# Kernel tuning notes

Measured on AMD Instinct MI355X. Metric: run time of the kernel, lower is better.

## Reference

```python
import jax, jax.numpy as jnp
import numpy as np

B, S, D, E, K = 4, 2048, 2048, 64, 2

def setup_inputs() -> dict:
    key = jax.random.key(0)
    k1, k2, k3, k4 = jax.random.split(key, 4)
    x = jax.random.normal(k1, (B, S, D), dtype=jnp.float32)
    W = jax.random.normal(k2, (E, D), dtype=jnp.float32) * 0.02  # gate_linear.weight
    noise_weight = jax.random.normal(k3, (E,), dtype=jnp.float32) * 0.02
    noise = jax.random.normal(k4, (B, S, E), dtype=jnp.float32)  # torch.randn_like(logits), noisy_std=1.0
    return {"x": x, "W": W, "noise_weight": noise_weight, "noise": noise, "k": K}

def reference(x, W, noise_weight, noise, k):
    # logits = x @ W.T  -> [B, S, E]
    logits = jnp.einsum('bsd,ed->bse', x, W)
    # noise injection: randn * noisy_std(=1.0) * noise_weight (per-expert scale)
    logits_noisy = logits + noise * noise_weight
    # top-k over experts
    top_vals, top_idx = jax.lax.top_k(logits_noisy, k)  # [B, S, k]
    # softmax over a tensor that is -inf everywhere except the top-k slots is
    # exactly: zeros everywhere, softmax(top_vals) scattered into the top-k slots.
    probs = jax.nn.softmax(top_vals, axis=-1)  # [B, S, k]
    n_tok = B * S
    rows = jnp.arange(n_tok)[:, None]  # [n_tok, 1]
    gated = jnp.zeros((n_tok, E), dtype=logits.dtype)
    gated = gated.at[rows, top_idx.reshape(n_tok, k)].set(probs.reshape(n_tok, k))
    gated = gated.reshape(B, S, E)
    return gated, top_idx, top_vals
```

## Files before the change

### kernel.cpp

```cpp
#include <hip/hip_runtime.h>
#include <math.h>

#define NTOK 8192
#define DDIM 2048
#define NEXP 64
#define MT   16
#define ASTR 136
#define CSTR 68

#define GATED_SZ (NTOK * NEXP)
#define IDX_OFF  GATED_SZ
#define VALS_OFF (GATED_SZ + NTOK * 2)

#define NKSTEP (DDIM / 32)
#define NTILE  (NEXP / 16)
#define BFRAG_HALVES ((size_t)NKSTEP * NTILE * 64 * 8)

typedef _Float16 f16x8 __attribute__((ext_vector_type(8)));
typedef float    f32x4 __attribute__((ext_vector_type(4)));

__global__ void pack_b_kernel(const float* __restrict__ W,
                              _Float16* __restrict__ Bh,
                              _Float16* __restrict__ Bl)
{
    const int tid  = blockIdx.x * blockDim.x + threadIdx.x;
    const int lane = tid & 63;
    const int fid  = tid >> 6;
    const int ks   = fid >> 2;
    const int nt   = fid & 3;
    const int e    = nt * 16 + (lane & 15);
    const int k    = ks * 32 + (lane >> 4) * 8;
    const float* src = W + (size_t)e * DDIM + k;

    f16x8 hi, lo;
#pragma unroll
    for (int j = 0; j < 8; ++j) {
        const float v = src[j];
        const _Float16 h = (_Float16)v;
        hi[j] = h;
        lo[j] = (_Float16)((v - (float)h) * 4096.f);
    }
    *(f16x8*)(Bh + (size_t)tid * 8) = hi;
    *(f16x8*)(Bl + (size_t)tid * 8) = lo;
}

#define BFRAG(base, ks, nt) \
    (*(const f16x8*)((base) + ((((size_t)(ks)) * 4 + (nt)) * 64 + lane) * 8))

static __device__ __forceinline__ void cvt_hilo(float4 v0, float4 v1,
                                                f16x8& h8, f16x8& l8)
{
    const float vv[8] = {v0.x, v0.y, v0.z, v0.w, v1.x, v1.y, v1.z, v1.w};
#pragma unroll
    for (int j = 0; j < 8; ++j) {
        const _Float16 hh = (_Float16)vv[j];
        h8[j] = hh;
        l8[j] = (_Float16)((vv[j] - (float)hh) * 4096.f);
    }
}

__global__ __launch_bounds__(512, 4) void gate_kernel(
    const float* __restrict__ x,
    const _Float16* __restrict__ Bh,
    const _Float16* __restrict__ Bl,
    const float* __restrict__ noise_w,
    const float* __restrict__ noise,
    float* __restrict__ out)
{
    __shared__ _Float16 smem[8 * 2 * MT * ASTR];

    const int tid  = threadIdx.x;
    const int lane = tid & 63;
    const int w    = __builtin_amdgcn_readfirstlane(tid >> 6);
    const int tokBase = blockIdx.x * MT;

    const int q = lane >> 4;
    const int m = lane & 15;

    _Float16* xs = smem + (size_t)w * (2 * MT * ASTR);

    const float* xw = x + (size_t)tokBase * DDIM + (size_t)w * 256;

    f32x4 acc_hh[4], acc_lo[4];
#pragma unroll
    for (int nt = 0; nt < 4; ++nt) {
        acc_hh[nt] = (f32x4){0.f, 0.f, 0.f, 0.f};
        acc_lo[nt] = (f32x4){0.f, 0.f, 0.f, 0.f};
    }

#define LOADSUB(sc)                                                          \
    _Pragma("unroll")                                                        \
    for (int p = 0; p < 4; ++p) {                                            \
        const float* src = xw + (size_t)(p * 4 + q) * DDIM + (sc) * 128 + m * 8; \
        s0[p] = *(const float4*)(src);                                       \
        s1[p] = *(const float4*)(src + 4);                                   \
    }

#define STAGESUB()                                                           \
    _Pragma("unroll")                                                        \
    for (int p = 0; p < 4; ++p) {                                            \
        f16x8 h8, l8;                                                        \
        cvt_hilo(s0[p], s1[p], h8, l8);                                      \
        const int off = (p * 4 + q) * ASTR + m * 8;                          \
        *(f16x8*)&xs[off] = h8;                                              \
        *(f16x8*)&xs[MT * ASTR + off] = l8;                                  \
    }

#define COMPUTESUB(sc)                                                       \
    _Pragma("unroll")                                                        \
    for (int stp = 0; stp < 4; ++stp) {                                      \
        const int ks = w * 8 + (sc) * 4 + stp;                               \
        const f16x8 ah = *(const f16x8*)&xs[m * ASTR + stp * 32 + q * 8];    \
        const f16x8 al = *(const f16x8*)&xs[MT * ASTR + m * ASTR + stp * 32 + q * 8]; \
        _Pragma("unroll")                                                    \
        for (int nt = 0; nt < 4; ++nt) {                                     \
            const f16x8 bh = BFRAG(Bh, ks, nt);                              \
            const f16x8 bl = BFRAG(Bl, ks, nt);                              \
            acc_hh[nt] = __builtin_amdgcn_mfma_f32_16x16x32_f16(ah, bh, acc_hh[nt], 0, 0, 0); \
            acc_lo[nt] = __builtin_amdgcn_mfma_f32_16x16x32_f16(ah, bl, acc_lo[nt], 0, 0, 0); \
            acc_lo[nt] = __builtin_amdgcn_mfma_f32_16x16x32_f16(al, bh, acc_lo[nt], 0, 0, 0); \
        }                                                                    \
    }

    float4 s0[4], s1[4];
    LOADSUB(0)
    STAGESUB()
    LOADSUB(1)
    COMPUTESUB(0)
    STAGESUB()
    COMPUTESUB(1)

#undef LOADSUB
#undef STAGESUB
#undef COMPUTESUB

    __syncthreads();
    float* cbuf = (float*)smem;

#pragma unroll
    for (int nt = 0; nt < 4; ++nt) {
        const int e = nt * 16 + m;
#pragma unroll
        for (int r = 0; r < 4; ++r) {
            const int t = q * 4 + r;
            cbuf[((w * MT) + t) * CSTR + e] = acc_hh[nt][r] + acc_lo[nt][r] * (1.f / 4096.f);
        }
    }
    __syncthreads();

    const float nwv = noise_w[lane];
#pragma unroll
    for (int i = 0; i < 2; ++i) {
        const int t   = w * 2 + i;
        const int tok = tokBase + t;
        const int e   = lane;

        float v = 0.f;
#pragma unroll
        for (int p = 0; p < 8; ++p)
            v += cbuf[((p * MT) + t) * CSTR + e];
        v += noise[(size_t)tok * NEXP + e] * nwv;

        float m1 = v; int i1 = e;
#pragma unroll
        for (int sh = 32; sh > 0; sh >>= 1) {
            float ov = __shfl_xor(m1, sh, 64);
            int   oi = __shfl_xor(i1, sh, 64);
            if (ov > m1 || (ov == m1 && oi < i1)) { m1 = ov; i1 = oi; }
        }
        float vm = (e == i1) ? -INFINITY : v;
        float m2 = vm; int i2 = e;
#pragma unroll
        for (int sh = 32; sh > 0; sh >>= 1) {
            float ov = __shfl_xor(m2, sh, 64);
            int   oi = __shfl_xor(i2, sh, 64);
            if (ov > m2 || (ov == m2 && oi < i2)) { m2 = ov; i2 = oi; }
        }

        const float e2  = expf(m2 - m1);
        const float inv = 1.f / (1.f + e2);
        const float p1  = inv;
        const float p2  = e2 * inv;

        float gval = 0.f;
        if (e == i1) gval = p1;
        else if (e == i2) gval = p2;
        out[(size_t)tok * NEXP + e] = gval;

        if (lane == 0) {
            out[IDX_OFF  + tok * 2 + 0] = (float)i1;
            out[IDX_OFF  + tok * 2 + 1] = (float)i2;
            out[VALS_OFF + tok * 2 + 0] = m1;
            out[VALS_OFF + tok * 2 + 1] = m2;
        }
    }
}

extern "C" void kernel_launch(void* const* d_in, const int* in_sizes, int n_in,
                              void* d_out, int out_size, void* d_ws, size_t ws_size,
                              hipStream_t stream) {
    const float* x     = (const float*)d_in[0];
    const float* W     = (const float*)d_in[1];
    const float* nw    = (const float*)d_in[2];
    const float* noise = (const float*)d_in[3];
    float* out = (float*)d_out;

    _Float16* Bh = (_Float16*)d_ws;
    _Float16* Bl = Bh + BFRAG_HALVES;

    hipLaunchKernelGGL(pack_b_kernel, dim3(64), dim3(256), 0, stream, W, Bh, Bl);

    hipLaunchKernelGGL(gate_kernel, dim3(NTOK / MT), dim3(512), 0, stream,
                       x, Bh, Bl, nw, noise, out);
}
```

Baseline: 112.0 us.

## Halve per-wave LDS staging and deepen x prefetch to four sub-chunks

Each wave now stages its 256-element K slice in four 64-wide sub-chunks instead of two 128-wide ones. This cuts the LDS row stride from 136 to 72 halves and roughly halves the block's shared memory, so more blocks can be resident per CU. Two float4 register buffers alternate, so two global loads of x stay in flight while the wave converts and computes the previous sub-chunk. The noise and noise_weight loads are also hoisted to kernel start so their latency hides behind the GEMM. The cost is more staging and compute phases with smaller MFMA batches between them.

```diff
diff --git a/kernel.cpp b/kernel.cpp
--- a/kernel.cpp
+++ b/kernel.cpp
@@ -5,7 +5,7 @@
 #define DDIM 2048
 #define NEXP 64
 #define MT   16
-#define ASTR 136
+#define ASTR 72
 #define CSTR 68
 
 #define GATED_SZ (NTOK * NEXP)
@@ -17,6 +17,7 @@
 #define BFRAG_HALVES ((size_t)NKSTEP * NTILE * 64 * 8)
 
 typedef _Float16 f16x8 __attribute__((ext_vector_type(8)));
+typedef _Float16 f16x4 __attribute__((ext_vector_type(4)));
 typedef float    f32x4 __attribute__((ext_vector_type(4)));
 
 __global__ void pack_b_kernel(const float* __restrict__ W,
@@ -47,15 +48,14 @@
 #define BFRAG(base, ks, nt) \
     (*(const f16x8*)((base) + ((((size_t)(ks)) * 4 + (nt)) * 64 + lane) * 8))
 
-static __device__ __forceinline__ void cvt_hilo(float4 v0, float4 v1,
-                                                f16x8& h8, f16x8& l8)
+static __device__ __forceinline__ void cvt_hilo4(float4 v, f16x4& h4, f16x4& l4)
 {
-    const float vv[8] = {v0.x, v0.y, v0.z, v0.w, v1.x, v1.y, v1.z, v1.w};
-#pragma unroll
-    for (int j = 0; j < 8; ++j) {
+    const float vv[4] = {v.x, v.y, v.z, v.w};
+#pragma unroll
+    for (int j = 0; j < 4; ++j) {
         const _Float16 hh = (_Float16)vv[j];
-        h8[j] = hh;
-        l8[j] = (_Float16)((vv[j] - (float)hh) * 4096.f);
+        h4[j] = hh;
+        l4[j] = (_Float16)((vv[j] - (float)hh) * 4096.f);
     }
 }
 
@@ -67,7 +67,7 @@
     const float* __restrict__ noise,
     float* __restrict__ out)
 {
-    __shared__ _Float16 smem[8 * 2 * MT * ASTR];
+    __shared__ __align__(16) char smem_raw[8 * 2 * MT * ASTR * 2];
 
     const int tid  = threadIdx.x;
     const int lane = tid & 63;
@@ -77,9 +77,13 @@
     const int q = lane >> 4;
     const int m = lane & 15;
 
-    _Float16* xs = smem + (size_t)w * (2 * MT * ASTR);
+    _Float16* xs = (_Float16*)smem_raw + (size_t)w * (2 * MT * ASTR);
 
     const float* xw = x + (size_t)tokBase * DDIM + (size_t)w * 256;
+
+    const float nwv = noise_w[lane];
+    const float nz0 = noise[(size_t)(tokBase + w * 2)     * NEXP + lane];
+    const float nz1 = noise[(size_t)(tokBase + w * 2 + 1) * NEXP + lane];
 
     f32x4 acc_hh[4], acc_lo[4];
 #pragma unroll
@@ -88,28 +92,27 @@
         acc_lo[nt] = (f32x4){0.f, 0.f, 0.f, 0.f};
     }
 
-#define LOADSUB(sc)                                                          \
+#define LOADSUB(buf, s)                                                      \
     _Pragma("unroll")                                                        \
     for (int p = 0; p < 4; ++p) {                                            \
-        const float* src = xw + (size_t)(p * 4 + q) * DDIM + (sc) * 128 + m * 8; \
-        s0[p] = *(const float4*)(src);                                       \
-        s1[p] = *(const float4*)(src + 4);                                   \
-    }
-
-#define STAGESUB()                                                           \
+        buf[p] = *(const float4*)(xw + (size_t)(p * 4 + q) * DDIM            \
+                                  + (s) * 64 + m * 4);                       \
+    }
+
+#define STAGESUB(buf)                                                        \
     _Pragma("unroll")                                                        \
     for (int p = 0; p < 4; ++p) {                                            \
-        f16x8 h8, l8;                                                        \
-        cvt_hilo(s0[p], s1[p], h8, l8);                                      \
-        const int off = (p * 4 + q) * ASTR + m * 8;                          \
-        *(f16x8*)&xs[off] = h8;                                              \
-        *(f16x8*)&xs[MT * ASTR + off] = l8;                                  \
-    }
-
-#define COMPUTESUB(sc)                                                       \
+        f16x4 h4, l4;                                                        \
+        cvt_hilo4(buf[p], h4, l4);                                           \
+        const int off = (p * 4 + q) * ASTR + m * 4;                          \
+        *(f16x4*)&xs[off] = h4;                                              \
+        *(f16x4*)&xs[MT * ASTR + off] = l4;                                  \
+    }
+
+#define COMPUTESUB(s)                                                        \
     _Pragma("unroll")                                                        \
-    for (int stp = 0; stp < 4; ++stp) {                                      \
-        const int ks = w * 8 + (sc) * 4 + stp;                               \
+    for (int stp = 0; stp < 2; ++stp) {                                      \
+        const int ks = w * 8 + (s) * 2 + stp;                                \
         const f16x8 ah = *(const f16x8*)&xs[m * ASTR + stp * 32 + q * 8];    \
         const f16x8 al = *(const f16x8*)&xs[MT * ASTR + m * ASTR + stp * 32 + q * 8]; \
         _Pragma("unroll")                                                    \
@@ -122,20 +125,26 @@
         }                                                                    \
     }
 
-    float4 s0[4], s1[4];
-    LOADSUB(0)
-    STAGESUB()
-    LOADSUB(1)
+    float4 rA[4], rB[4];
+    LOADSUB(rA, 0)
+    LOADSUB(rB, 1)
+    STAGESUB(rA)
+    LOADSUB(rA, 2)
     COMPUTESUB(0)
-    STAGESUB()
+    STAGESUB(rB)
+    LOADSUB(rB, 3)
     COMPUTESUB(1)
+    STAGESUB(rA)
+    COMPUTESUB(2)
+    STAGESUB(rB)
+    COMPUTESUB(3)
 
 #undef LOADSUB
 #undef STAGESUB
 #undef COMPUTESUB
 
     __syncthreads();
-    float* cbuf = (float*)smem;
+    float* cbuf = (float*)smem_raw;
 
 #pragma unroll
     for (int nt = 0; nt < 4; ++nt) {
@@ -148,7 +157,6 @@
     }
     __syncthreads();
 
-    const float nwv = noise_w[lane];
 #pragma unroll
     for (int i = 0; i < 2; ++i) {
         const int t   = w * 2 + i;
@@ -159,7 +167,7 @@
 #pragma unroll
         for (int p = 0; p < 8; ++p)
             v += cbuf[((p * MT) + t) * CSTR + e];
-        v += noise[(size_t)tok * NEXP + e] * nwv;
+        v += (i ? nz1 : nz0) * nwv;
 
         float m1 = v; int i1 = e;
 #pragma unroll
```

Measured after the change: 112.8 us. Within noise of the previous version (+0.7%).
